# Performance work log

Measured on AMD Instinct MI355X. Metric: run time of the kernel, lower is better.

The kernel has to match this reference:

```python
import jax, jax.numpy as jnp
import numpy as np

N_NODES = 50000
N_EDGES = 800000
IN_FEAT = 4
HIDDEN = 128
NUM_LAYERS = 3


def setup_inputs() -> dict:
    key = jax.random.key(0)
    ks = jax.random.split(key, 16)
    x = jax.random.normal(ks[0], (N_NODES, IN_FEAT), dtype=jnp.float32)
    edge_index = jax.random.randint(ks[1], (2, N_EDGES), 0, N_NODES, dtype=jnp.int64)

    def lin(k, fan_in, fan_out):
        bound = 1.0 / np.sqrt(fan_in)
        k1, k2 = jax.random.split(k)
        W = jax.random.uniform(k1, (fan_in, fan_out), minval=-bound, maxval=bound, dtype=jnp.float32)
        b = jax.random.uniform(k2, (fan_out,), minval=-bound, maxval=bound, dtype=jnp.float32)
        return W, b

    W_enc, b_enc = lin(ks[2], IN_FEAT, HIDDEN)
    W_g1, b_g1 = lin(ks[3], HIDDEN, HIDDEN)
    W_g2, b_g2 = lin(ks[4], HIDDEN, HIDDEN)
    W_g3, b_g3 = lin(ks[5], HIDDEN, HIDDEN)
    W_m1, b_m1 = lin(ks[6], 2 * HIDDEN, HIDDEN)
    W_m2, b_m2 = lin(ks[7], HIDDEN, 3)
    return {
        "x": x, "edge_index": edge_index,
        "W_enc": W_enc, "b_enc": b_enc,
        "W_g1": W_g1, "b_g1": b_g1,
        "W_g2": W_g2, "b_g2": b_g2,
        "W_g3": W_g3, "b_g3": b_g3,
        "W_m1": W_m1, "b_m1": b_m1,
        "W_m2": W_m2, "b_m2": b_m2,
    }


def _gcn_forward(x, edge_index, W_enc, b_enc, gcn_params, W_m1, b_m1, W_m2, b_m2):
    n = x.shape[0]
    # Node encoder (linear + ReLU) -> [N, H]
    h = jax.nn.relu(x @ W_enc + b_enc)

    # Add self-loops once (GCNConv default add_self_loops=True)
    src = jnp.concatenate([edge_index[0], jnp.arange(n, dtype=edge_index.dtype)])
    dst = jnp.concatenate([edge_index[1], jnp.arange(n, dtype=edge_index.dtype)])
    # Symmetric degree normalization: D^{-1/2} (A+I) D^{-1/2}
    deg = jax.ops.segment_sum(jnp.ones_like(dst, dtype=h.dtype), dst, num_segments=n)
    deg_inv_sqrt = jnp.where(deg > 0, jax.lax.rsqrt(jnp.maximum(deg, 1.0)), 0.0)
    norm = (deg_inv_sqrt[src] * deg_inv_sqrt[dst])[:, None]  # [E+N, 1]

    for (W, b) in gcn_params:
        m = (h @ W)[src] * norm                       # gather + scale messages
        h = jax.ops.segment_sum(m, dst, num_segments=n) + b
        h = jax.nn.relu(h)                            # dropout is identity at eval

    # Edge classifier: gather endpoints, concat, MLP -> [E, 3]
    ef = jnp.concatenate([h[edge_index[0]], h[edge_index[1]]], axis=-1)
    return jax.nn.relu(ef @ W_m1 + b_m1) @ W_m2 + b_m2


def reference(x, edge_index, W_enc, b_enc, W_g1, b_g1, W_g2, b_g2, W_g3, b_g3, W_m1, b_m1, W_m2, b_m2):
    gcn_params = [(W_g1, b_g1), (W_g2, b_g2), (W_g3, b_g3)]
    return _gcn_forward(x, edge_index, W_enc, b_enc, gcn_params, W_m1, b_m1, W_m2, b_m2)
```

## Files before the change

kernel.cpp:

```cpp
#include <hip/hip_runtime.h>
#include <hip/hip_bf16.h>

#define N_NODES 50000
#define N_EDGES 800000
#define HID 128
#define SCAN_BLK 512
#define N_SCAN_BLOCKS ((N_NODES + SCAN_BLK - 1) / SCAN_BLK)

typedef __attribute__((ext_vector_type(8))) short bf16x8;
typedef __attribute__((ext_vector_type(4))) float f32x4;

__device__ __forceinline__ ushort f2bf(float f) {
    uint u = __float_as_uint(f);
    return (ushort)((u + 0x7FFFu + ((u >> 16) & 1u)) >> 16);
}
__device__ __forceinline__ float bf2f(ushort h) { return __uint_as_float(((uint)h) << 16); }

__global__ void k_count(const int* __restrict__ ei, int* cnt) {
    int e = blockIdx.x * blockDim.x + threadIdx.x;
    if (e < N_EDGES) atomicAdd(&cnt[ei[N_EDGES + e]], 1);
}

__global__ __launch_bounds__(SCAN_BLK) void k_scan1(const int* __restrict__ cnt,
                                                    int* __restrict__ rowStart,
                                                    int* __restrict__ blockSums,
                                                    float* __restrict__ dinv) {
    __shared__ int tmp[SCAN_BLK];
    int i = blockIdx.x * SCAN_BLK + threadIdx.x;
    int v = (i < N_NODES) ? cnt[i] : 0;
    if (i < N_NODES) dinv[i] = rsqrtf(1.0f + (float)v);
    tmp[threadIdx.x] = v;
    __syncthreads();
    for (int off = 1; off < SCAN_BLK; off <<= 1) {
        int t = (threadIdx.x >= off) ? tmp[threadIdx.x - off] : 0;
        __syncthreads();
        tmp[threadIdx.x] += t;
        __syncthreads();
    }
    if (i < N_NODES) rowStart[i] = tmp[threadIdx.x] - v;
    if (threadIdx.x == SCAN_BLK - 1) blockSums[blockIdx.x] = tmp[SCAN_BLK - 1];
}

__global__ __launch_bounds__(SCAN_BLK) void k_scan23(int* __restrict__ rowStart,
                                                     const int* __restrict__ blockSums,
                                                     int* __restrict__ cursor) {
    __shared__ int ps[128];
    int t = threadIdx.x;
    if (t < 128) ps[t] = (t < N_SCAN_BLOCKS) ? blockSums[t] : 0;
    __syncthreads();
    for (int off = 1; off < 128; off <<= 1) {
        int v = (t < 128 && t >= off) ? ps[t - off] : 0;
        __syncthreads();
        if (t < 128) ps[t] += v;
        __syncthreads();
    }
    int i = blockIdx.x * SCAN_BLK + t;
    int prefix = (blockIdx.x == 0) ? 0 : ps[blockIdx.x - 1];
    if (i < N_NODES) {
        rowStart[i] += prefix;
        cursor[i] = 0;
    }
    if (i == 0) rowStart[N_NODES] = N_EDGES;
}

__global__ void k_fill(const int* __restrict__ ei, const int* __restrict__ rowStart,
                       int* cursor, int2* __restrict__ csrE) {
    int e = blockIdx.x * blockDim.x + threadIdx.x;
    if (e < N_EDGES) {
        int s = ei[e];
        int d = ei[N_EDGES + e];
        int pos = rowStart[d] + atomicAdd(&cursor[d], 1);
        csrE[pos] = make_int2(s, e);
    }
}

struct WSplitArgs {
    const float* src[5];
    ushort* th[5];
    ushort* tl[5];
};

__global__ void k_tsplit5(WSplitArgs a) {
    int i = blockIdx.x * 256 + threadIdx.x;
    int which = i >> 14, r = i & 16383;
    int k = r >> 7, j = r & 127;
    float v = a.src[which][r];
    ushort hi = f2bf(v);
    a.th[which][j * 128 + k] = hi;
    a.tl[which][j * 128 + k] = f2bf(v - bf2f(hi));
}

__global__ void k_encoder(const float* __restrict__ x, const float* __restrict__ W,
                          const float* __restrict__ b, ushort* __restrict__ hH,
                          ushort* __restrict__ hL) {
    int i = blockIdx.x * 256 + threadIdx.x;
    int n = i >> 6, l = i & 63;
    int j = l * 2;
    float4 xv = *(const float4*)(x + (size_t)n * 4);
    float2 acc = *(const float2*)(b + j);
    float2 w0 = *(const float2*)(W + 0 * 128 + j);
    float2 w1 = *(const float2*)(W + 1 * 128 + j);
    float2 w2 = *(const float2*)(W + 2 * 128 + j);
    float2 w3 = *(const float2*)(W + 3 * 128 + j);
    acc.x += xv.x * w0.x + xv.y * w1.x + xv.z * w2.x + xv.w * w3.x;
    acc.y += xv.x * w0.y + xv.y * w1.y + xv.z * w2.y + xv.w * w3.y;
    float v0 = fmaxf(acc.x, 0.f), v1 = fmaxf(acc.y, 0.f);
    ushort h0 = f2bf(v0), h1 = f2bf(v1);
    ushort l0 = f2bf(v0 - bf2f(h0)), l1 = f2bf(v1 - bf2f(h1));
    ((uint*)hH)[i] = (uint)h0 | ((uint)h1 << 16);
    ((uint*)hL)[i] = (uint)l0 | ((uint)l1 << 16);
}

__device__ __forceinline__ void gemm_body(const ushort* __restrict__ AH,
                                          const ushort* __restrict__ AL,
                                          const ushort* __restrict__ BTH,
                                          const ushort* __restrict__ BTL,
                                          float* __restrict__ out,
                                          const float* __restrict__ bias,
                                          const float* __restrict__ scale, int M) {
    int tid = threadIdx.x;
    int w = tid >> 6, l = tid & 63;
    int ln = l & 15, lk = l >> 4;
    int r0 = blockIdx.x * 128 + w * 32;
    int row0 = r0 + ln, row1 = r0 + 16 + ln;
    int a0 = row0 < M ? row0 : M - 1;
    int a1 = row1 < M ? row1 : M - 1;

    f32x4 acc0[8] = {};
    f32x4 acc1[8] = {};
#pragma unroll
    for (int kc = 0; kc < 4; ++kc) {
        int ko = kc * 32 + lk * 8;
        bf16x8 h0H = *(const bf16x8*)(AH + (size_t)a0 * 128 + ko);
        bf16x8 h0L = *(const bf16x8*)(AL + (size_t)a0 * 128 + ko);
        bf16x8 h1H = *(const bf16x8*)(AH + (size_t)a1 * 128 + ko);
        bf16x8 h1L = *(const bf16x8*)(AL + (size_t)a1 * 128 + ko);
#pragma unroll
        for (int nt = 0; nt < 8; ++nt) {
            size_t boff = (size_t)(nt * 16 + ln) * 128 + ko;
            bf16x8 wH = *(const bf16x8*)(BTH + boff);
            bf16x8 wL = *(const bf16x8*)(BTL + boff);
            acc0[nt] = __builtin_amdgcn_mfma_f32_16x16x32_bf16(wH, h0H, acc0[nt], 0, 0, 0);
            acc0[nt] = __builtin_amdgcn_mfma_f32_16x16x32_bf16(wL, h0H, acc0[nt], 0, 0, 0);
            acc0[nt] = __builtin_amdgcn_mfma_f32_16x16x32_bf16(wH, h0L, acc0[nt], 0, 0, 0);
            acc1[nt] = __builtin_amdgcn_mfma_f32_16x16x32_bf16(wH, h1H, acc1[nt], 0, 0, 0);
            acc1[nt] = __builtin_amdgcn_mfma_f32_16x16x32_bf16(wL, h1H, acc1[nt], 0, 0, 0);
            acc1[nt] = __builtin_amdgcn_mfma_f32_16x16x32_bf16(wH, h1L, acc1[nt], 0, 0, 0);
        }
    }
    float s0v = scale ? scale[a0] : 1.f;
    float s1v = scale ? scale[a1] : 1.f;
#pragma unroll
    for (int nt = 0; nt < 8; ++nt) {
        int jb = nt * 16 + lk * 4;
        float4 bv;
        if (bias) bv = *(const float4*)(bias + jb);
        else bv = make_float4(0.f, 0.f, 0.f, 0.f);
        if (row0 < M) {
            float4 o = make_float4((acc0[nt][0] + bv.x) * s0v, (acc0[nt][1] + bv.y) * s0v,
                                   (acc0[nt][2] + bv.z) * s0v, (acc0[nt][3] + bv.w) * s0v);
            *(float4*)(out + (size_t)row0 * 128 + jb) = o;
        }
        if (row1 < M) {
            float4 o = make_float4((acc1[nt][0] + bv.x) * s1v, (acc1[nt][1] + bv.y) * s1v,
                                   (acc1[nt][2] + bv.z) * s1v, (acc1[nt][3] + bv.w) * s1v);
            *(float4*)(out + (size_t)row1 * 128 + jb) = o;
        }
    }
}

__global__ __launch_bounds__(256) void k_gemm_mfma(const ushort* __restrict__ AH,
                                                   const ushort* __restrict__ AL,
                                                   const ushort* __restrict__ BTH,
                                                   const ushort* __restrict__ BTL,
                                                   float* __restrict__ out,
                                                   const float* __restrict__ scale, int M) {
    gemm_body(AH, AL, BTH, BTL, out, nullptr, scale, M);
}

__global__ __launch_bounds__(256) void k_gemm_pq(const ushort* __restrict__ AH,
                                                 const ushort* __restrict__ AL,
                                                 const ushort* __restrict__ BTHt,
                                                 const ushort* __restrict__ BTLt,
                                                 const ushort* __restrict__ BTHb,
                                                 const ushort* __restrict__ BTLb,
                                                 float* __restrict__ outP,
                                                 float* __restrict__ outQ,
                                                 const float* __restrict__ b1, int M) {
    if (blockIdx.y == 0)
        gemm_body(AH, AL, BTHt, BTLt, outP, nullptr, nullptr, M);
    else
        gemm_body(AH, AL, BTHb, BTLb, outQ, b1, nullptr, M);
}

__global__ __launch_bounds__(256) void k_aggregate(const float* __restrict__ hw,
                                                   const float* __restrict__ b,
                                                   const float* __restrict__ dinv,
                                                   const int* __restrict__ rowStart,
                                                   const int2* __restrict__ csrE,
                                                   ushort* __restrict__ hH,
                                                   ushort* __restrict__ hL) {
    int wid = (blockIdx.x * 256 + threadIdx.x) >> 6;
    int l = threadIdx.x & 63;
    if (wid >= N_NODES) return;
    int g = l >> 4, li = l & 15;
    int c8 = li * 8;

    float4 aA, aB;
    if (g == 0) {
        aA = *(const float4*)(hw + (size_t)wid * 128 + c8);
        aB = *(const float4*)(hw + (size_t)wid * 128 + c8 + 4);
    } else {
        aA = make_float4(0.f, 0.f, 0.f, 0.f);
        aB = aA;
    }

    int s0 = rowStart[wid], s1 = rowStart[wid + 1];
    int k = s0 + g;
    float4 v0a = make_float4(0.f, 0.f, 0.f, 0.f), v0b = v0a;
    if (k < s1) {
        const float* r = hw + (size_t)csrE[k].x * 128 + c8;
        v0a = *(const float4*)(r);
        v0b = *(const float4*)(r + 4);
    }
    for (; k < s1; k += 4) {
        float4 v1a = make_float4(0.f, 0.f, 0.f, 0.f), v1b = v1a;
        if (k + 4 < s1) {
            const float* r = hw + (size_t)csrE[k + 4].x * 128 + c8;
            v1a = *(const float4*)(r);
            v1b = *(const float4*)(r + 4);
        }
        aA.x += v0a.x; aA.y += v0a.y; aA.z += v0a.z; aA.w += v0a.w;
        aB.x += v0b.x; aB.y += v0b.y; aB.z += v0b.z; aB.w += v0b.w;
        v0a = v1a;
        v0b = v1b;
    }
    aA.x += __shfl_xor(aA.x, 16); aA.y += __shfl_xor(aA.y, 16);
    aA.z += __shfl_xor(aA.z, 16); aA.w += __shfl_xor(aA.w, 16);
    aB.x += __shfl_xor(aB.x, 16); aB.y += __shfl_xor(aB.y, 16);
    aB.z += __shfl_xor(aB.z, 16); aB.w += __shfl_xor(aB.w, 16);
    aA.x += __shfl_xor(aA.x, 32); aA.y += __shfl_xor(aA.y, 32);
    aA.z += __shfl_xor(aA.z, 32); aA.w += __shfl_xor(aA.w, 32);
    aB.x += __shfl_xor(aB.x, 32); aB.y += __shfl_xor(aB.y, 32);
    aB.z += __shfl_xor(aB.z, 32); aB.w += __shfl_xor(aB.w, 32);

    if (g == 0) {
        float di = dinv[wid];
        float4 bbA = *(const float4*)(b + c8);
        float4 bbB = *(const float4*)(b + c8 + 4);
        float f0 = fmaxf(bbA.x + di * aA.x, 0.f);
        float f1 = fmaxf(bbA.y + di * aA.y, 0.f);
        float f2 = fmaxf(bbA.z + di * aA.z, 0.f);
        float f3 = fmaxf(bbA.w + di * aA.w, 0.f);
        float f4v = fmaxf(bbB.x + di * aB.x, 0.f);
        float f5 = fmaxf(bbB.y + di * aB.y, 0.f);
        float f6 = fmaxf(bbB.z + di * aB.z, 0.f);
        float f7 = fmaxf(bbB.w + di * aB.w, 0.f);
        ushort h0 = f2bf(f0), h1 = f2bf(f1), h2 = f2bf(f2), h3 = f2bf(f3);
        ushort h4 = f2bf(f4v), h5 = f2bf(f5), h6 = f2bf(f6), h7 = f2bf(f7);
        uint4 uh = make_uint4((uint)h0 | ((uint)h1 << 16), (uint)h2 | ((uint)h3 << 16),
                              (uint)h4 | ((uint)h5 << 16), (uint)h6 | ((uint)h7 << 16));
        ushort l0 = f2bf(f0 - bf2f(h0)), l1 = f2bf(f1 - bf2f(h1));
        ushort l2 = f2bf(f2 - bf2f(h2)), l3 = f2bf(f3 - bf2f(h3));
        ushort l4 = f2bf(f4v - bf2f(h4)), l5 = f2bf(f5 - bf2f(h5));
        ushort l6 = f2bf(f6 - bf2f(h6)), l7 = f2bf(f7 - bf2f(h7));
        uint4 ul = make_uint4((uint)l0 | ((uint)l1 << 16), (uint)l2 | ((uint)l3 << 16),
                              (uint)l4 | ((uint)l5 << 16), (uint)l6 | ((uint)l7 << 16));
        *(uint4*)(hH + (size_t)wid * 128 + c8) = uh;
        *(uint4*)(hL + (size_t)wid * 128 + c8) = ul;
    }
}

__global__ __launch_bounds__(256) void k_edge_final(const float* __restrict__ P,
                                                    const float* __restrict__ Qb,
                                                    const int* __restrict__ rowStart,
                                                    const int2* __restrict__ csrE,
                                                    const float* __restrict__ W2,
                                                    const float* __restrict__ b2,
                                                    float* __restrict__ out) {
    int wid = (blockIdx.x * 256 + threadIdx.x) >> 6;
    int l = threadIdx.x & 63;
    if (wid >= N_NODES) return;
    int s0 = rowStart[wid], s1 = rowStart[wid + 1];
    if (s0 >= s1) return;
    int j8 = (l & 15) * 8;
    int g = l >> 4;

    float4 qa = *(const float4*)(Qb + (size_t)wid * 128 + j8);
    float4 qb = *(const float4*)(Qb + (size_t)wid * 128 + j8 + 4);
    float w2r[8][3];
#pragma unroll
    for (int k = 0; k < 8; ++k) {
        w2r[k][0] = W2[(j8 + k) * 3 + 0];
        w2r[k][1] = W2[(j8 + k) * 3 + 1];
        w2r[k][2] = W2[(j8 + k) * 3 + 2];
    }
    float bz0 = b2[0], bz1 = b2[1], bz2 = b2[2];

    int k = s0 + g;
    int2 c = make_int2(0, 0);
    float4 pa = make_float4(0.f, 0.f, 0.f, 0.f), pb = pa;
    if (k < s1) {
        c = csrE[k];
        const float* pr = P + (size_t)c.x * 128 + j8;
        pa = *(const float4*)(pr);
        pb = *(const float4*)(pr + 4);
    }
    for (; k < s1; k += 4) {
        int kn = k + 4;
        int2 cn = make_int2(0, 0);
        float4 pan = make_float4(0.f, 0.f, 0.f, 0.f), pbn = pan;
        if (kn < s1) {
            cn = csrE[kn];
            const float* prn = P + (size_t)cn.x * 128 + j8;
            pan = *(const float4*)(prn);
            pbn = *(const float4*)(prn + 4);
        }
        float z[8];
        z[0] = fmaxf(pa.x + qa.x, 0.f);
        z[1] = fmaxf(pa.y + qa.y, 0.f);
        z[2] = fmaxf(pa.z + qa.z, 0.f);
        z[3] = fmaxf(pa.w + qa.w, 0.f);
        z[4] = fmaxf(pb.x + qb.x, 0.f);
        z[5] = fmaxf(pb.y + qb.y, 0.f);
        z[6] = fmaxf(pb.z + qb.z, 0.f);
        z[7] = fmaxf(pb.w + qb.w, 0.f);
        float o0 = 0.f, o1 = 0.f, o2 = 0.f;
#pragma unroll
        for (int q = 0; q < 8; ++q) {
            o0 += z[q] * w2r[q][0];
            o1 += z[q] * w2r[q][1];
            o2 += z[q] * w2r[q][2];
        }
#pragma unroll
        for (int m = 1; m < 16; m <<= 1) {
            o0 += __shfl_xor(o0, m);
            o1 += __shfl_xor(o1, m);
            o2 += __shfl_xor(o2, m);
        }
        if ((l & 15) == 0) {
            float* op = out + (size_t)c.y * 3;
            op[0] = o0 + bz0;
            op[1] = o1 + bz1;
            op[2] = o2 + bz2;
        }
        c = cn;
        pa = pan;
        pb = pbn;
    }
}

extern "C" void kernel_launch(void* const* d_in, const int* in_sizes, int n_in,
                              void* d_out, int out_size, void* d_ws, size_t ws_size,
                              hipStream_t stream) {
    const float* x     = (const float*)d_in[0];
    const int*   ei    = (const int*)d_in[1];
    const float* W_enc = (const float*)d_in[2];
    const float* b_enc = (const float*)d_in[3];
    const float* Wg[3] = {(const float*)d_in[4], (const float*)d_in[6], (const float*)d_in[8]};
    const float* bg[3] = {(const float*)d_in[5], (const float*)d_in[7], (const float*)d_in[9]};
    const float* W_m1  = (const float*)d_in[10];
    const float* b_m1  = (const float*)d_in[11];
    const float* W_m2  = (const float*)d_in[12];
    const float* b_m2  = (const float*)d_in[13];
    float* out = (float*)d_out;

    char* w = (char*)d_ws;
    ushort* hH      = (ushort*)w;  w += (size_t)N_NODES * HID * 2;
    ushort* hL      = (ushort*)w;  w += (size_t)N_NODES * HID * 2;
    float*  hB      = (float*)w;   w += (size_t)N_NODES * HID * 4;
    float*  Qb      = (float*)w;   w += (size_t)N_NODES * HID * 4;
    int2*   csrE    = (int2*)w;    w += (size_t)N_EDGES * 8;
    float*  dinv    = (float*)w;   w += (size_t)N_NODES * 4;
    int*    rowStart= (int*)w;     w += (size_t)(N_NODES + 4) * 4;
    int*    cursor  = (int*)w;     w += (size_t)N_NODES * 4;
    int*    blockSums=(int*)w;     w += 512;
    ushort* WgTH[3], *WgTL[3];
    for (int i = 0; i < 3; ++i) {
        WgTH[i] = (ushort*)w; w += 128 * 128 * 2;
        WgTL[i] = (ushort*)w; w += 128 * 128 * 2;
    }
    ushort* WtTH = (ushort*)w; w += 128 * 128 * 2;
    ushort* WtTL = (ushort*)w; w += 128 * 128 * 2;
    ushort* WbTH = (ushort*)w; w += 128 * 128 * 2;
    ushort* WbTL = (ushort*)w; w += 128 * 128 * 2;

    hipMemsetAsync(cursor, 0, (size_t)N_NODES * 4, stream);
    k_count<<<(N_EDGES + 255) / 256, 256, 0, stream>>>(ei, cursor);
    k_scan1<<<N_SCAN_BLOCKS, SCAN_BLK, 0, stream>>>(cursor, rowStart, blockSums, dinv);
    k_scan23<<<N_SCAN_BLOCKS, SCAN_BLK, 0, stream>>>(rowStart, blockSums, cursor);
    k_fill<<<(N_EDGES + 255) / 256, 256, 0, stream>>>(ei, rowStart, cursor, csrE);

    WSplitArgs wa;
    wa.src[0] = Wg[0]; wa.th[0] = WgTH[0]; wa.tl[0] = WgTL[0];
    wa.src[1] = Wg[1]; wa.th[1] = WgTH[1]; wa.tl[1] = WgTL[1];
    wa.src[2] = Wg[2]; wa.th[2] = WgTH[2]; wa.tl[2] = WgTL[2];
    wa.src[3] = W_m1;             wa.th[3] = WtTH; wa.tl[3] = WtTL;
    wa.src[4] = W_m1 + 128 * 128; wa.th[4] = WbTH; wa.tl[4] = WbTL;
    k_tsplit5<<<5 * 16384 / 256, 256, 0, stream>>>(wa);

    k_encoder<<<N_NODES * 64 / 256, 256, 0, stream>>>(x, W_enc, b_enc, hH, hL);

    const int gemmGrid = (N_NODES + 127) / 128;
    for (int l = 0; l < 3; ++l) {
        k_gemm_mfma<<<gemmGrid, 256, 0, stream>>>(hH, hL, WgTH[l], WgTL[l], hB, dinv, N_NODES);
        k_aggregate<<<(N_NODES * 64) / 256, 256, 0, stream>>>(hB, bg[l], dinv, rowStart, csrE, hH, hL);
    }

    dim3 pqGrid(gemmGrid, 2);
    k_gemm_pq<<<pqGrid, 256, 0, stream>>>(hH, hL, WtTH, WtTL, WbTH, WbTL, hB, Qb, b_m1, N_NODES);

    k_edge_final<<<(N_NODES * 64) / 256, 256, 0, stream>>>(hB, Qb, rowStart, csrE, W_m2, b_m2, out);
}
```

Before: 469.3 us.

## Fuse GCN aggregation with next layer's MFMA GEMM via shared-memory tile

Replaces the separate aggregate and GEMM kernels with a fused kernel. Each 512-thread block aggregates 16 nodes, writes the bf16 hi/lo split to LDS, and immediately multiplies by the next weight matrix (or by both edge-MLP halves on the final layer). This removes the hH/hL round trip through global memory and several launches. In exchange, each wave multiplies only one 16-column tile, so every block re-reads the weights from global or L2. The grid also assumes N_NODES is divisible by 16.

```diff
diff --git a/kernel.cpp b/kernel.cpp
--- a/kernel.cpp
+++ b/kernel.cpp
@@ -111,13 +111,12 @@
     ((uint*)hL)[i] = (uint)l0 | ((uint)l1 << 16);
 }
 
-__device__ __forceinline__ void gemm_body(const ushort* __restrict__ AH,
-                                          const ushort* __restrict__ AL,
-                                          const ushort* __restrict__ BTH,
-                                          const ushort* __restrict__ BTL,
-                                          float* __restrict__ out,
-                                          const float* __restrict__ bias,
-                                          const float* __restrict__ scale, int M) {
+__global__ __launch_bounds__(256) void k_gemm_mfma(const ushort* __restrict__ AH,
+                                                   const ushort* __restrict__ AL,
+                                                   const ushort* __restrict__ BTH,
+                                                   const ushort* __restrict__ BTL,
+                                                   float* __restrict__ out,
+                                                   const float* __restrict__ scale, int M) {
     int tid = threadIdx.x;
     int w = tid >> 6, l = tid & 63;
     int ln = l & 15, lk = l >> 4;
@@ -148,126 +147,145 @@
             acc1[nt] = __builtin_amdgcn_mfma_f32_16x16x32_bf16(wH, h1L, acc1[nt], 0, 0, 0);
         }
     }
-    float s0v = scale ? scale[a0] : 1.f;
-    float s1v = scale ? scale[a1] : 1.f;
+    float s0v = scale[a0];
+    float s1v = scale[a1];
 #pragma unroll
     for (int nt = 0; nt < 8; ++nt) {
         int jb = nt * 16 + lk * 4;
-        float4 bv;
-        if (bias) bv = *(const float4*)(bias + jb);
-        else bv = make_float4(0.f, 0.f, 0.f, 0.f);
         if (row0 < M) {
-            float4 o = make_float4((acc0[nt][0] + bv.x) * s0v, (acc0[nt][1] + bv.y) * s0v,
-                                   (acc0[nt][2] + bv.z) * s0v, (acc0[nt][3] + bv.w) * s0v);
+            float4 o = make_float4(acc0[nt][0] * s0v, acc0[nt][1] * s0v,
+                                   acc0[nt][2] * s0v, acc0[nt][3] * s0v);
             *(float4*)(out + (size_t)row0 * 128 + jb) = o;
         }
         if (row1 < M) {
-            float4 o = make_float4((acc1[nt][0] + bv.x) * s1v, (acc1[nt][1] + bv.y) * s1v,
-                                   (acc1[nt][2] + bv.z) * s1v, (acc1[nt][3] + bv.w) * s1v);
+            float4 o = make_float4(acc1[nt][0] * s1v, acc1[nt][1] * s1v,
+                                   acc1[nt][2] * s1v, acc1[nt][3] * s1v);
             *(float4*)(out + (size_t)row1 * 128 + jb) = o;
         }
     }
 }
 
-__global__ __launch_bounds__(256) void k_gemm_mfma(const ushort* __restrict__ AH,
-                                                   const ushort* __restrict__ AL,
-                                                   const ushort* __restrict__ BTH,
-                                                   const ushort* __restrict__ BTL,
-                                                   float* __restrict__ out,
-                                                   const float* __restrict__ scale, int M) {
-    gemm_body(AH, AL, BTH, BTL, out, nullptr, scale, M);
-}
-
-__global__ __launch_bounds__(256) void k_gemm_pq(const ushort* __restrict__ AH,
-                                                 const ushort* __restrict__ AL,
-                                                 const ushort* __restrict__ BTHt,
-                                                 const ushort* __restrict__ BTLt,
-                                                 const ushort* __restrict__ BTHb,
-                                                 const ushort* __restrict__ BTLb,
-                                                 float* __restrict__ outP,
-                                                 float* __restrict__ outQ,
-                                                 const float* __restrict__ b1, int M) {
-    if (blockIdx.y == 0)
-        gemm_body(AH, AL, BTHt, BTLt, outP, nullptr, nullptr, M);
-    else
-        gemm_body(AH, AL, BTHb, BTLb, outQ, b1, nullptr, M);
-}
-
-__global__ __launch_bounds__(256) void k_aggregate(const float* __restrict__ hw,
-                                                   const float* __restrict__ b,
-                                                   const float* __restrict__ dinv,
-                                                   const int* __restrict__ rowStart,
-                                                   const int2* __restrict__ csrE,
-                                                   ushort* __restrict__ hH,
-                                                   ushort* __restrict__ hL) {
-    int wid = (blockIdx.x * 256 + threadIdx.x) >> 6;
-    int l = threadIdx.x & 63;
-    if (wid >= N_NODES) return;
+__global__ __launch_bounds__(512, 8) void k_agg_gemm(
+    const float* __restrict__ hw, const float* __restrict__ bg,
+    const float* __restrict__ dinv, const int* __restrict__ rowStart,
+    const int2* __restrict__ csrE,
+    const ushort* __restrict__ BTH1, const ushort* __restrict__ BTL1,
+    const ushort* __restrict__ BTH2, const ushort* __restrict__ BTL2,
+    float* __restrict__ out1, float* __restrict__ out2,
+    const float* __restrict__ b1, const float* __restrict__ outScale) {
+    __shared__ uint AsH[16][64];
+    __shared__ uint AsL[16][64];
+    int tid = threadIdx.x;
+    int w = tid >> 6, l = tid & 63;
     int g = l >> 4, li = l & 15;
     int c8 = li * 8;
 
-    float4 aA, aB;
-    if (g == 0) {
-        aA = *(const float4*)(hw + (size_t)wid * 128 + c8);
-        aB = *(const float4*)(hw + (size_t)wid * 128 + c8 + 4);
+#pragma unroll
+    for (int q = 0; q < 2; ++q) {
+        int n = blockIdx.x * 16 + w * 2 + q;
+        float4 aA, aB;
+        if (g == 0) {
+            aA = *(const float4*)(hw + (size_t)n * 128 + c8);
+            aB = *(const float4*)(hw + (size_t)n * 128 + c8 + 4);
+        } else {
+            aA = make_float4(0.f, 0.f, 0.f, 0.f);
+            aB = aA;
+        }
+        int s0 = rowStart[n], s1 = rowStart[n + 1];
+        int k = s0 + g;
+        float4 v0a = make_float4(0.f, 0.f, 0.f, 0.f), v0b = v0a;
+        if (k < s1) {
+            const float* r = hw + (size_t)csrE[k].x * 128 + c8;
+            v0a = *(const float4*)(r);
+            v0b = *(const float4*)(r + 4);
+        }
+        for (; k < s1; k += 4) {
+            float4 v1a = make_float4(0.f, 0.f, 0.f, 0.f), v1b = v1a;
+            if (k + 4 < s1) {
+                const float* r = hw + (size_t)csrE[k + 4].x * 128 + c8;
+                v1a = *(const float4*)(r);
+                v1b = *(const float4*)(r + 4);
+            }
+            aA.x += v0a.x; aA.y += v0a.y; aA.z += v0a.z; aA.w += v0a.w;
+            aB.x += v0b.x; aB.y += v0b.y; aB.z += v0b.z; aB.w += v0b.w;
+            v0a = v1a;
+            v0b = v1b;
+        }
+        aA.x += __shfl_xor(aA.x, 16); aA.y += __shfl_xor(aA.y, 16);
+        aA.z += __shfl_xor(aA.z, 16); aA.w += __shfl_xor(aA.w, 16);
+        aB.x += __shfl_xor(aB.x, 16); aB.y += __shfl_xor(aB.y, 16);
+        aB.z += __shfl_xor(aB.z, 16); aB.w += __shfl_xor(aB.w, 16);
+        aA.x += __shfl_xor(aA.x, 32); aA.y += __shfl_xor(aA.y, 32);
+        aA.z += __shfl_xor(aA.z, 32); aA.w += __shfl_xor(aA.w, 32);
+        aB.x += __shfl_xor(aB.x, 32); aB.y += __shfl_xor(aB.y, 32);
+        aB.z += __shfl_xor(aB.z, 32); aB.w += __shfl_xor(aB.w, 32);
+
+        if (g == 0) {
+            float di = dinv[n];
+            float4 bbA = *(const float4*)(bg + c8);
+            float4 bbB = *(const float4*)(bg + c8 + 4);
+            float f0 = fmaxf(bbA.x + di * aA.x, 0.f);
+            float f1 = fmaxf(bbA.y + di * aA.y, 0.f);
+            float f2 = fmaxf(bbA.z + di * aA.z, 0.f);
+            float f3 = fmaxf(bbA.w + di * aA.w, 0.f);
+            float f4 = fmaxf(bbB.x + di * aB.x, 0.f);
+            float f5 = fmaxf(bbB.y + di * aB.y, 0.f);
+            float f6 = fmaxf(bbB.z + di * aB.z, 0.f);
+            float f7 = fmaxf(bbB.w + di * aB.w, 0.f);
+            ushort h0 = f2bf(f0), h1 = f2bf(f1), h2 = f2bf(f2), h3 = f2bf(f3);
+            ushort h4 = f2bf(f4), h5 = f2bf(f5), h6 = f2bf(f6), h7 = f2bf(f7);
+            uint4 uh = make_uint4((uint)h0 | ((uint)h1 << 16), (uint)h2 | ((uint)h3 << 16),
+                                  (uint)h4 | ((uint)h5 << 16), (uint)h6 | ((uint)h7 << 16));
+            ushort l0 = f2bf(f0 - bf2f(h0)), l1 = f2bf(f1 - bf2f(h1));
+            ushort l2 = f2bf(f2 - bf2f(h2)), l3 = f2bf(f3 - bf2f(h3));
+            ushort l4 = f2bf(f4 - bf2f(h4)), l5 = f2bf(f5 - bf2f(h5));
+            ushort l6 = f2bf(f6 - bf2f(h6)), l7 = f2bf(f7 - bf2f(h7));
+            uint4 ul = make_uint4((uint)l0 | ((uint)l1 << 16), (uint)l2 | ((uint)l3 << 16),
+                                  (uint)l4 | ((uint)l5 << 16), (uint)l6 | ((uint)l7 << 16));
+            int r = w * 2 + q;
+            *(uint4*)&AsH[r][li * 4] = uh;
+            *(uint4*)&AsL[r][li * 4] = ul;
+        }
+    }
+    __syncthreads();
+
+    int ln = l & 15, lk = l >> 4;
+    int ct = w;
+    int node = blockIdx.x * 16 + ln;
+    f32x4 acc1 = {};
+    f32x4 acc2 = {};
+#pragma unroll
+    for (int kc = 0; kc < 4; ++kc) {
+        uint4 uh = *(uint4*)&AsH[ln][kc * 16 + lk * 4];
+        uint4 ul = *(uint4*)&AsL[ln][kc * 16 + lk * 4];
+        bf16x8 hh, hl;
+        __builtin_memcpy(&hh, &uh, 16);
+        __builtin_memcpy(&hl, &ul, 16);
+        size_t boff = (size_t)(ct * 16 + ln) * 128 + kc * 32 + lk * 8;
+        bf16x8 wh = *(const bf16x8*)(BTH1 + boff);
+        bf16x8 wl = *(const bf16x8*)(BTL1 + boff);
+        acc1 = __builtin_amdgcn_mfma_f32_16x16x32_bf16(wh, hh, acc1, 0, 0, 0);
+        acc1 = __builtin_amdgcn_mfma_f32_16x16x32_bf16(wl, hh, acc1, 0, 0, 0);
+        acc1 = __builtin_amdgcn_mfma_f32_16x16x32_bf16(wh, hl, acc1, 0, 0, 0);
+        if (BTH2) {
+            bf16x8 wh2 = *(const bf16x8*)(BTH2 + boff);
+            bf16x8 wl2 = *(const bf16x8*)(BTL2 + boff);
+            acc2 = __builtin_amdgcn_mfma_f32_16x16x32_bf16(wh2, hh, acc2, 0, 0, 0);
+            acc2 = __builtin_amdgcn_mfma_f32_16x16x32_bf16(wl2, hh, acc2, 0, 0, 0);
+            acc2 = __builtin_amdgcn_mfma_f32_16x16x32_bf16(wh2, hl, acc2, 0, 0, 0);
+        }
+    }
+    int jb = ct * 16 + lk * 4;
+    if (outScale) {
+        float s = outScale[node];
+        *(float4*)(out1 + (size_t)node * 128 + jb) =
+            make_float4(acc1[0] * s, acc1[1] * s, acc1[2] * s, acc1[3] * s);
     } else {
-        aA = make_float4(0.f, 0.f, 0.f, 0.f);
-        aB = aA;
-    }
-
-    int s0 = rowStart[wid], s1 = rowStart[wid + 1];
-    int k = s0 + g;
-    float4 v0a = make_float4(0.f, 0.f, 0.f, 0.f), v0b = v0a;
-    if (k < s1) {
-        const float* r = hw + (size_t)csrE[k].x * 128 + c8;
-        v0a = *(const float4*)(r);
-        v0b = *(const float4*)(r + 4);
-    }
-    for (; k < s1; k += 4) {
-        float4 v1a = make_float4(0.f, 0.f, 0.f, 0.f), v1b = v1a;
-        if (k + 4 < s1) {
-            const float* r = hw + (size_t)csrE[k + 4].x * 128 + c8;
-            v1a = *(const float4*)(r);
-            v1b = *(const float4*)(r + 4);
-        }
-        aA.x += v0a.x; aA.y += v0a.y; aA.z += v0a.z; aA.w += v0a.w;
-        aB.x += v0b.x; aB.y += v0b.y; aB.z += v0b.z; aB.w += v0b.w;
-        v0a = v1a;
-        v0b = v1b;
-    }
-    aA.x += __shfl_xor(aA.x, 16); aA.y += __shfl_xor(aA.y, 16);
-    aA.z += __shfl_xor(aA.z, 16); aA.w += __shfl_xor(aA.w, 16);
-    aB.x += __shfl_xor(aB.x, 16); aB.y += __shfl_xor(aB.y, 16);
-    aB.z += __shfl_xor(aB.z, 16); aB.w += __shfl_xor(aB.w, 16);
-    aA.x += __shfl_xor(aA.x, 32); aA.y += __shfl_xor(aA.y, 32);
-    aA.z += __shfl_xor(aA.z, 32); aA.w += __shfl_xor(aA.w, 32);
-    aB.x += __shfl_xor(aB.x, 32); aB.y += __shfl_xor(aB.y, 32);
-    aB.z += __shfl_xor(aB.z, 32); aB.w += __shfl_xor(aB.w, 32);
-
-    if (g == 0) {
-        float di = dinv[wid];
-        float4 bbA = *(const float4*)(b + c8);
-        float4 bbB = *(const float4*)(b + c8 + 4);
-        float f0 = fmaxf(bbA.x + di * aA.x, 0.f);
-        float f1 = fmaxf(bbA.y + di * aA.y, 0.f);
-        float f2 = fmaxf(bbA.z + di * aA.z, 0.f);
-        float f3 = fmaxf(bbA.w + di * aA.w, 0.f);
-        float f4v = fmaxf(bbB.x + di * aB.x, 0.f);
-        float f5 = fmaxf(bbB.y + di * aB.y, 0.f);
-        float f6 = fmaxf(bbB.z + di * aB.z, 0.f);
-        float f7 = fmaxf(bbB.w + di * aB.w, 0.f);
-        ushort h0 = f2bf(f0), h1 = f2bf(f1), h2 = f2bf(f2), h3 = f2bf(f3);
-        ushort h4 = f2bf(f4v), h5 = f2bf(f5), h6 = f2bf(f6), h7 = f2bf(f7);
-        uint4 uh = make_uint4((uint)h0 | ((uint)h1 << 16), (uint)h2 | ((uint)h3 << 16),
-                              (uint)h4 | ((uint)h5 << 16), (uint)h6 | ((uint)h7 << 16));
-        ushort l0 = f2bf(f0 - bf2f(h0)), l1 = f2bf(f1 - bf2f(h1));
-        ushort l2 = f2bf(f2 - bf2f(h2)), l3 = f2bf(f3 - bf2f(h3));
-        ushort l4 = f2bf(f4v - bf2f(h4)), l5 = f2bf(f5 - bf2f(h5));
-        ushort l6 = f2bf(f6 - bf2f(h6)), l7 = f2bf(f7 - bf2f(h7));
-        uint4 ul = make_uint4((uint)l0 | ((uint)l1 << 16), (uint)l2 | ((uint)l3 << 16),
-                              (uint)l4 | ((uint)l5 << 16), (uint)l6 | ((uint)l7 << 16));
-        *(uint4*)(hH + (size_t)wid * 128 + c8) = uh;
-        *(uint4*)(hL + (size_t)wid * 128 + c8) = ul;
+        *(float4*)(out1 + (size_t)node * 128 + jb) =
+            make_float4(acc1[0], acc1[1], acc1[2], acc1[3]);
+        float4 bv = *(const float4*)(b1 + jb);
+        *(float4*)(out2 + (size_t)node * 128 + jb) =
+            make_float4(acc2[0] + bv.x, acc2[1] + bv.y, acc2[2] + bv.z, acc2[3] + bv.w);
     }
 }
 
@@ -368,8 +386,8 @@
     char* w = (char*)d_ws;
     ushort* hH      = (ushort*)w;  w += (size_t)N_NODES * HID * 2;
     ushort* hL      = (ushort*)w;  w += (size_t)N_NODES * HID * 2;
-    float*  hB      = (float*)w;   w += (size_t)N_NODES * HID * 4;
-    float*  Qb      = (float*)w;   w += (size_t)N_NODES * HID * 4;
+    float*  bufA    = (float*)w;   w += (size_t)N_NODES * HID * 4;
+    float*  bufB    = (float*)w;   w += (size_t)N_NODES * HID * 4;
     int2*   csrE    = (int2*)w;    w += (size_t)N_EDGES * 8;
     float*  dinv    = (float*)w;   w += (size_t)N_NODES * 4;
     int*    rowStart= (int*)w;     w += (size_t)(N_NODES + 4) * 4;
@@ -385,6 +403,9 @@
     ushort* WbTH = (ushort*)w; w += 128 * 128 * 2;
     ushort* WbTL = (ushort*)w; w += 128 * 128 * 2;
 
+    float* P  = (float*)hH;
+    float* Qb = bufB;
+
     hipMemsetAsync(cursor, 0, (size_t)N_NODES * 4, stream);
     k_count<<<(N_EDGES + 255) / 256, 256, 0, stream>>>(ei, cursor);
     k_scan1<<<N_SCAN_BLOCKS, SCAN_BLK, 0, stream>>>(cursor, rowStart, blockSums, dinv);
@@ -401,14 +422,18 @@
 
     k_encoder<<<N_NODES * 64 / 256, 256, 0, stream>>>(x, W_enc, b_enc, hH, hL);
 
-    const int gemmGrid = (N_NODES + 127) / 128;
-    for (int l = 0; l < 3; ++l) {
-        k_gemm_mfma<<<gemmGrid, 256, 0, stream>>>(hH, hL, WgTH[l], WgTL[l], hB, dinv, N_NODES);
-        k_aggregate<<<(N_NODES * 64) / 256, 256, 0, stream>>>(hB, bg[l], dinv, rowStart, csrE, hH, hL);
-    }
-
-    dim3 pqGrid(gemmGrid, 2);
-    k_gemm_pq<<<pqGrid, 256, 0, stream>>>(hH, hL, WtTH, WtTL, WbTH, WbTL, hB, Qb, b_m1, N_NODES);
-
-    k_edge_final<<<(N_NODES * 64) / 256, 256, 0, stream>>>(hB, Qb, rowStart, csrE, W_m2, b_m2, out);
-}
+    k_gemm_mfma<<<(N_NODES + 127) / 128, 256, 0, stream>>>(hH, hL, WgTH[0], WgTL[0], bufA, dinv, N_NODES);
+
+    const int fusedGrid = N_NODES / 16;
+    k_agg_gemm<<<fusedGrid, 512, 0, stream>>>(bufA, bg[0], dinv, rowStart, csrE,
+                                              WgTH[1], WgTL[1], nullptr, nullptr,
+                                              bufB, nullptr, nullptr, dinv);
+    k_agg_gemm<<<fusedGrid, 512, 0, stream>>>(bufB, bg[1], dinv, rowStart, csrE,
+                                              WgTH[2], WgTL[2], nullptr, nullptr,
+                                              bufA, nullptr, nullptr, dinv);
+    k_agg_gemm<<<fusedGrid, 512, 0, stream>>>(bufA, bg[2], dinv, rowStart, csrE,
+                                              WtTH, WtTL, WbTH, WbTL,
+                                              P, Qb, b_m1, nullptr);
+
+    k_edge_final<<<(N_NODES * 64) / 256, 256, 0, stream>>>(P, Qb, rowStart, csrE, W_m2, b_m2, out);
+}
```

After: 477.3 us. No clear change (+1.7%).
